# Kernel tuning notes

Measured on AMD Instinct MI355X. Metric: run time of the kernel, lower is better.

The kernel has to match this reference:

```python
import jax, jax.numpy as jnp
import numpy as np

B, N, M, E = 2, 16384, 16384, 49152
W_CHAMFER, W_EDGE = 1.0, 0.1


def setup_inputs() -> dict:
    key = jax.random.key(0)
    k1, k2, k3 = jax.random.split(key, 3)
    pred_verts = jax.random.normal(k1, (B, N, 3), dtype=jnp.float32)
    target_verts = jax.random.normal(k2, (B, M, 3), dtype=jnp.float32)
    edges = jax.random.randint(k3, (E, 2), 0, N, dtype=jnp.int64)
    return {"pred_verts": pred_verts, "target_verts": target_verts, "edges": edges}


def reference(pred_verts, target_verts, edges):
    # --- Chamfer distance (torch.cdist + bidirectional min) ---
    # Squared-distance expansion avoids materializing the B x N x M x 3 diff tensor.
    p2 = jnp.sum(pred_verts * pred_verts, axis=-1)            # [B, N]
    t2 = jnp.sum(target_verts * target_verts, axis=-1)        # [B, M]
    cross = jnp.einsum('bnd,bmd->bnm', pred_verts, target_verts)  # [B, N, M]
    d2 = p2[:, :, None] + t2[:, None, :] - 2.0 * cross
    dist = jnp.sqrt(jnp.maximum(d2, 0.0))                     # [B, N, M]
    c_loss = jnp.mean(jnp.min(dist, axis=2)) + jnp.mean(jnp.min(dist, axis=1))

    # --- Edge-length variance regularization (vectorized over batch) ---
    v1 = pred_verts[:, edges[:, 0]]                           # [B, E, 3]
    v2 = pred_verts[:, edges[:, 1]]                           # [B, E, 3]
    edge_lengths = jnp.linalg.norm(v1 - v2, axis=-1)          # [B, E]
    # torch.var defaults to unbiased (ddof=1); mean over batch == sum/B
    e_loss = jnp.mean(jnp.var(edge_lengths, axis=1, ddof=1))

    total_loss = W_CHAMFER * c_loss + W_EDGE * e_loss
    return (total_loss, c_loss, e_loss)
```

## Files before the change

kernel.cpp:

```cpp
#include <hip/hip_runtime.h>
#include <float.h>

#define B_SZ 2
#define N_SZ 16384
#define E_SZ 49152

#define TPB 512
#define WAVES (TPB / 64)
#define ROWS_PER_BLOCK 256
#define MSPLIT 4
#define MRANGE (N_SZ / MSPLIT)
#define CHUNK 512
#define NCHUNK (MRANGE / CHUNK)
#define TILES_PER_CHUNK (CHUNK / 32)

#define CH_BLOCKS (2 * (B_SZ * N_SZ / ROWS_PER_BLOCK) * MSPLIT)
#define EDGE_BLOCKS (B_SZ * E_SZ / TPB)
#define NROWS_TOT (2 * B_SZ * N_SZ)

#define PLANE_BYTES (N_SZ * 16)
#define BATCH_FRAG_BYTES (2 * PLANE_BYTES)
#define DIR_FRAG_BYTES (B_SZ * BATCH_FRAG_BYTES)
#define MINS_OFF (2 * DIR_FRAG_BYTES)
#define SUMS_OFF (MINS_OFF + NROWS_TOT * 4)

typedef short short8 __attribute__((ext_vector_type(8)));
typedef float f32x16 __attribute__((ext_vector_type(16)));

__device__ inline short f2bf(float f) {
    unsigned u = __float_as_uint(f);
    unsigned r = (u + 0x7fffu + ((u >> 16) & 1u)) >> 16;
    return (short)r;
}
__device__ inline float bf2f(short s) {
    return __uint_as_float(((unsigned)(unsigned short)s) << 16);
}

__device__ inline unsigned fmapu(float f) {
    unsigned u = __float_as_uint(f);
    return ((int)u < 0) ? ~u : (u ^ 0x80000000u);
}
__device__ inline float funmapu(unsigned v) {
    unsigned b = ((int)v < 0) ? (v ^ 0x80000000u) : ~v;
    return __uint_as_float(b);
}

__global__ __launch_bounds__(TPB) void prep(const float* __restrict__ pred,
                                            const float* __restrict__ tgt,
                                            char* __restrict__ ws) {
    int idx = blockIdx.x * TPB + threadIdx.x;
    if (blockIdx.x == 0 && threadIdx.x < 6)
        ((double*)(ws + SUMS_OFF))[threadIdx.x] = 0.0;
    if (idx < NROWS_TOT) ((unsigned*)(ws + MINS_OFF))[idx] = 0xFFFFFFFFu;
    if (idx >= 2 * B_SZ * N_SZ) return;

    const bool isTgt = idx < B_SZ * N_SZ;
    int row = isTgt ? idx : idx - B_SZ * N_SZ;
    int batch = row >> 14, pt = row & (N_SZ - 1);
    const float* src = (isTgt ? tgt : pred) + (size_t)row * 3;
    char* base = ws + (isTgt ? 0 : DIR_FRAG_BYTES) + (size_t)batch * BATCH_FRAG_BYTES;

    float tx = src[0], ty = src[1], tz = src[2];
    short hx = f2bf(tx), hy = f2bf(ty), hz = f2bf(tz);
    short lx = f2bf(tx - bf2f(hx)), ly = f2bf(ty - bf2f(hy)), lz = f2bf(tz - bf2f(hz));
    float t2 = fmaf(tx, tx, fmaf(ty, ty, tz * tz));
    short t2h = f2bf(t2), t2l = f2bf(t2 - bf2f(t2h));
    const short one = 0x3f80;

    *(short8*)(base + (size_t)pt * 16) = (short8){hx, hy, hz, hx, hy, hz, one, one};
    *(short8*)(base + PLANE_BYTES + (size_t)pt * 16) =
        (short8){lx, ly, lz, t2h, t2l, 0, 0, 0};
}

__global__ __launch_bounds__(TPB, 1) void main_kernel(
    const float* __restrict__ pred, const float* __restrict__ tgt,
    const int* __restrict__ edges, char* __restrict__ ws)
{
    __shared__ __align__(16) char sB[2][2 * CHUNK * 16];
    __shared__ float wred[WAVES], wred2[WAVES];
    double* sums = (double*)(ws + SUMS_OFF);
    unsigned* minOut = (unsigned*)(ws + MINS_OFF);
    const int lane = threadIdx.x & 63;
    const int wv = threadIdx.x >> 6;

    if (blockIdx.x >= EDGE_BLOCKS) {
        const int cb = blockIdx.x - EDGE_BLOCKS;
        const int dir = cb >> 9;
        const int rest = cb & 511;
        const int ms = rest >> 7;
        const int xb = rest & 127;
        const int batch = xb >> 6;
        const int rowInB = (xb & 63) * ROWS_PER_BLOCK;
        const float* P = dir ? tgt : pred;
        const char* fragBase = ws + (size_t)dir * DIR_FRAG_BYTES
                                  + (size_t)batch * BATCH_FRAG_BYTES;
        const int mBase = ms * MRANGE;
        const int bl = lane & 31;
        const int half = lane >> 5;

        int r = batch * N_SZ + rowInB + wv * 32 + bl;
        const float* p = P + (size_t)r * 3;
        float px = p[0], py = p[1], pz = p[2];
        float ax = -2.f * px, ay = -2.f * py, az = -2.f * pz;
        short ahx = f2bf(ax), ahy = f2bf(ay), ahz = f2bf(az);
        short alx = f2bf(ax - bf2f(ahx)), aly = f2bf(ay - bf2f(ahy)),
              alz = f2bf(az - bf2f(ahz));
        float p2 = fmaf(px, px, fmaf(py, py, pz * pz));
        short p2h = f2bf(p2), p2l = f2bf(p2 - bf2f(p2h));
        const short one = 0x3f80;
        short8 af = half == 0
            ? (short8){ahx, ahy, ahz, alx, aly, alz, p2h, p2l}
            : (short8){ahx, ahy, ahz, one, one, 0, 0, 0};

        const int t = threadIdx.x;
        float4 st0, st1;
        auto ldChunk = [&](int c) {
            const float4* s0 = (const float4*)(fragBase + (size_t)(mBase + c * CHUNK) * 16);
            const float4* s1 = (const float4*)(fragBase + PLANE_BYTES
                                               + (size_t)(mBase + c * CHUNK) * 16);
            st0 = s0[t]; st1 = s1[t];
        };
        auto wrChunk = [&](int buf) {
            float4* d = (float4*)sB[buf];
            d[t] = st0; d[t + TPB] = st1;
        };

        float nmin[16];
        #pragma unroll
        for (int e = 0; e < 16; e++) nmin[e] = FLT_MAX;
        const f32x16 zc = {0.f, 0.f, 0.f, 0.f, 0.f, 0.f, 0.f, 0.f,
                           0.f, 0.f, 0.f, 0.f, 0.f, 0.f, 0.f, 0.f};

        ldChunk(0); wrChunk(0);
        __syncthreads();

        for (int c = 0; c < NCHUNK; c++) {
            int buf = c & 1;
            if (c + 1 < NCHUNK) ldChunk(c + 1);
            const char* bp = sB[buf] + half * (CHUNK * 16) + bl * 16;
            #pragma unroll 2
            for (int mt = 0; mt < TILES_PER_CHUNK; mt += 2) {
                short8 b0 = *(const short8*)(bp + (mt * 32) * 16);
                short8 b1 = *(const short8*)(bp + (mt * 32 + 32) * 16);
                f32x16 r0 = __builtin_amdgcn_mfma_f32_32x32x16_bf16(af, b0, zc, 0, 0, 0);
                f32x16 r1 = __builtin_amdgcn_mfma_f32_32x32x16_bf16(af, b1, zc, 0, 0, 0);
                #pragma unroll
                for (int e = 0; e < 16; e++)
                    nmin[e] = fminf(fminf(r0[e], r1[e]), nmin[e]);
            }
            if (c + 1 < NCHUNK) wrChunk(buf ^ 1);
            __syncthreads();
        }

        float vals[16];
        #pragma unroll
        for (int e = 0; e < 16; e++) {
            float v = nmin[e];
            v = fminf(v, __shfl_xor(v, 1));
            v = fminf(v, __shfl_xor(v, 2));
            v = fminf(v, __shfl_xor(v, 4));
            v = fminf(v, __shfl_xor(v, 8));
            v = fminf(v, __shfl_xor(v, 16));
            vals[e] = v;
        }
        if (bl == 0) {
            int base = dir * (B_SZ * N_SZ) + batch * N_SZ + rowInB + wv * 32 + half * 4;
            #pragma unroll
            for (int e = 0; e < 16; e++) {
                int rrow = (e & 3) + 8 * (e >> 2);
                atomicMin(&minOut[base + rrow], fmapu(vals[e]));
            }
        }
    } else {
        int idx = blockIdx.x * TPB + threadIdx.x;
        int b = idx >= E_SZ;
        int e = idx - b * E_SZ;
        int2 ee = ((const int2*)edges)[e];
        const float* p0 = pred + ((size_t)b * N_SZ + (size_t)ee.x) * 3;
        const float* p1 = pred + ((size_t)b * N_SZ + (size_t)ee.y) * 3;
        float dx = p0[0] - p1[0], dy = p0[1] - p1[1], dz = p0[2] - p1[2];
        float len = sqrtf(dx * dx + dy * dy + dz * dz);
        float s = len, q = len * len;
        for (int o = 32; o > 0; o >>= 1) {
            s += __shfl_down(s, o, 64);
            q += __shfl_down(q, o, 64);
        }
        if (lane == 0) { wred[wv] = s; wred2[wv] = q; }
        __syncthreads();
        if (threadIdx.x == 0) {
            float ts = 0.f, tq = 0.f;
            #pragma unroll
            for (int w = 0; w < WAVES; w++) { ts += wred[w]; tq += wred2[w]; }
            atomicAdd(&sums[2 + 2 * b], (double)ts);
            atomicAdd(&sums[3 + 2 * b], (double)tq);
        }
    }
}

#define FIN_TPB 1024
__global__ __launch_bounds__(FIN_TPB) void final_kernel(const char* __restrict__ ws,
                                                        float* __restrict__ out) {
    const uint4* mins = (const uint4*)(ws + MINS_OFF);
    const double* sums = (const double*)(ws + SUMS_OFF);
    __shared__ double redA[FIN_TPB / 64], redB[FIN_TPB / 64];

    float sA = 0.f, sB = 0.f;
    #pragma unroll
    for (int i = 0; i < 16; i++) {
        uint4 v = mins[i * FIN_TPB + threadIdx.x];
        float s = sqrtf(fmaxf(funmapu(v.x), 0.f)) + sqrtf(fmaxf(funmapu(v.y), 0.f))
                + sqrtf(fmaxf(funmapu(v.z), 0.f)) + sqrtf(fmaxf(funmapu(v.w), 0.f));
        if (i < 8) sA += s; else sB += s;
    }
    for (int o = 32; o > 0; o >>= 1) {
        sA += __shfl_down(sA, o, 64);
        sB += __shfl_down(sB, o, 64);
    }
    int wv = threadIdx.x >> 6, ln = threadIdx.x & 63;
    if (ln == 0) { redA[wv] = (double)sA; redB[wv] = (double)sB; }
    __syncthreads();
    if (threadIdx.x == 0) {
        double tA = 0.0, tB = 0.0;
        #pragma unroll
        for (int w = 0; w < FIN_TPB / 64; w++) { tA += redA[w]; tB += redB[w]; }
        double c = tA / (double)(B_SZ * N_SZ) + tB / (double)(B_SZ * N_SZ);
        double e = 0.0;
        #pragma unroll
        for (int b = 0; b < B_SZ; b++) {
            double s = sums[2 + 2 * b], q = sums[3 + 2 * b];
            e += (q - s * s / (double)E_SZ) / (double)(E_SZ - 1);
        }
        e *= (1.0 / B_SZ);
        double tot = 1.0 * c + 0.1 * e;
        out[0] = (float)tot;
        out[1] = (float)c;
        out[2] = (float)e;
    }
}

extern "C" void kernel_launch(void* const* d_in, const int* in_sizes, int n_in,
                              void* d_out, int out_size, void* d_ws, size_t ws_size,
                              hipStream_t stream) {
    const float* pred = (const float*)d_in[0];
    const float* tgt  = (const float*)d_in[1];
    const int* edges  = (const int*)d_in[2];
    float* out = (float*)d_out;
    char* ws = (char*)d_ws;

    prep<<<dim3((2 * B_SZ * N_SZ) / TPB), TPB, 0, stream>>>(pred, tgt, ws);

    main_kernel<<<dim3(EDGE_BLOCKS + CH_BLOCKS), TPB, 0, stream>>>(
        pred, tgt, edges, ws);

    final_kernel<<<dim3(1), FIN_TPB, 0, stream>>>(ws, out);
}
```

Before: 110.0 us.

## Give each wave two row tiles sharing one B fragment per MFMA pair

The chamfer block size drops to 256 threads, and each wave now handles 64 rows as two 32-row A fragments. Each B fragment loaded from LDS feeds two MFMAs, which halves LDS reads per MFMA and doubles register-held minima. The chunk loader now stages four float4s per thread to fill the same shared buffer with fewer threads. The prep kernel keeps its 512-thread config. Edge blocks also become 256 threads, so EDGE_BLOCKS doubles and the block-index decoding may be affected.

```diff
diff --git a/kernel.cpp b/kernel.cpp
--- a/kernel.cpp
+++ b/kernel.cpp
@@ -5,7 +5,7 @@
 #define N_SZ 16384
 #define E_SZ 49152
 
-#define TPB 512
+#define TPB 256
 #define WAVES (TPB / 64)
 #define ROWS_PER_BLOCK 256
 #define MSPLIT 4
@@ -45,10 +45,10 @@
     return __uint_as_float(b);
 }
 
-__global__ __launch_bounds__(TPB) void prep(const float* __restrict__ pred,
+__global__ __launch_bounds__(512) void prep(const float* __restrict__ pred,
                                             const float* __restrict__ tgt,
                                             char* __restrict__ ws) {
-    int idx = blockIdx.x * TPB + threadIdx.x;
+    int idx = blockIdx.x * 512 + threadIdx.x;
     if (blockIdx.x == 0 && threadIdx.x < 6)
         ((double*)(ws + SUMS_OFF))[threadIdx.x] = 0.0;
     if (idx < NROWS_TOT) ((unsigned*)(ws + MINS_OFF))[idx] = 0xFFFFFFFFu;
@@ -97,37 +97,42 @@
         const int mBase = ms * MRANGE;
         const int bl = lane & 31;
         const int half = lane >> 5;
-
-        int r = batch * N_SZ + rowInB + wv * 32 + bl;
-        const float* p = P + (size_t)r * 3;
-        float px = p[0], py = p[1], pz = p[2];
-        float ax = -2.f * px, ay = -2.f * py, az = -2.f * pz;
-        short ahx = f2bf(ax), ahy = f2bf(ay), ahz = f2bf(az);
-        short alx = f2bf(ax - bf2f(ahx)), aly = f2bf(ay - bf2f(ahy)),
-              alz = f2bf(az - bf2f(ahz));
-        float p2 = fmaf(px, px, fmaf(py, py, pz * pz));
-        short p2h = f2bf(p2), p2l = f2bf(p2 - bf2f(p2h));
         const short one = 0x3f80;
-        short8 af = half == 0
-            ? (short8){ahx, ahy, ahz, alx, aly, alz, p2h, p2l}
-            : (short8){ahx, ahy, ahz, one, one, 0, 0, 0};
+
+        const int rowLocal = rowInB + wv * 64;
+        short8 af[2];
+        #pragma unroll
+        for (int t = 0; t < 2; t++) {
+            int r = batch * N_SZ + rowLocal + t * 32 + bl;
+            const float* p = P + (size_t)r * 3;
+            float px = p[0], py = p[1], pz = p[2];
+            float ax = -2.f * px, ay = -2.f * py, az = -2.f * pz;
+            short ahx = f2bf(ax), ahy = f2bf(ay), ahz = f2bf(az);
+            short alx = f2bf(ax - bf2f(ahx)), aly = f2bf(ay - bf2f(ahy)),
+                  alz = f2bf(az - bf2f(ahz));
+            float p2 = fmaf(px, px, fmaf(py, py, pz * pz));
+            short p2h = f2bf(p2), p2l = f2bf(p2 - bf2f(p2h));
+            af[t] = half == 0
+                ? (short8){ahx, ahy, ahz, alx, aly, alz, p2h, p2l}
+                : (short8){ahx, ahy, ahz, one, one, 0, 0, 0};
+        }
 
         const int t = threadIdx.x;
-        float4 st0, st1;
+        float4 st0, st1, st2, st3;
         auto ldChunk = [&](int c) {
             const float4* s0 = (const float4*)(fragBase + (size_t)(mBase + c * CHUNK) * 16);
             const float4* s1 = (const float4*)(fragBase + PLANE_BYTES
                                                + (size_t)(mBase + c * CHUNK) * 16);
-            st0 = s0[t]; st1 = s1[t];
+            st0 = s0[t]; st1 = s0[t + TPB]; st2 = s1[t]; st3 = s1[t + TPB];
         };
         auto wrChunk = [&](int buf) {
             float4* d = (float4*)sB[buf];
-            d[t] = st0; d[t + TPB] = st1;
+            d[t] = st0; d[t + TPB] = st1; d[t + 2 * TPB] = st2; d[t + 3 * TPB] = st3;
         };
 
-        float nmin[16];
-        #pragma unroll
-        for (int e = 0; e < 16; e++) nmin[e] = FLT_MAX;
+        float nmin0[16], nmin1[16];
+        #pragma unroll
+        for (int e = 0; e < 16; e++) { nmin0[e] = FLT_MAX; nmin1[e] = FLT_MAX; }
         const f32x16 zc = {0.f, 0.f, 0.f, 0.f, 0.f, 0.f, 0.f, 0.f,
                            0.f, 0.f, 0.f, 0.f, 0.f, 0.f, 0.f, 0.f};
 
@@ -139,36 +144,36 @@
             if (c + 1 < NCHUNK) ldChunk(c + 1);
             const char* bp = sB[buf] + half * (CHUNK * 16) + bl * 16;
             #pragma unroll 2
-            for (int mt = 0; mt < TILES_PER_CHUNK; mt += 2) {
+            for (int mt = 0; mt < TILES_PER_CHUNK; mt++) {
                 short8 b0 = *(const short8*)(bp + (mt * 32) * 16);
-                short8 b1 = *(const short8*)(bp + (mt * 32 + 32) * 16);
-                f32x16 r0 = __builtin_amdgcn_mfma_f32_32x32x16_bf16(af, b0, zc, 0, 0, 0);
-                f32x16 r1 = __builtin_amdgcn_mfma_f32_32x32x16_bf16(af, b1, zc, 0, 0, 0);
+                f32x16 r0 = __builtin_amdgcn_mfma_f32_32x32x16_bf16(af[0], b0, zc, 0, 0, 0);
+                f32x16 r1 = __builtin_amdgcn_mfma_f32_32x32x16_bf16(af[1], b0, zc, 0, 0, 0);
                 #pragma unroll
-                for (int e = 0; e < 16; e++)
-                    nmin[e] = fminf(fminf(r0[e], r1[e]), nmin[e]);
+                for (int e = 0; e < 16; e++) {
+                    nmin0[e] = fminf(nmin0[e], r0[e]);
+                    nmin1[e] = fminf(nmin1[e], r1[e]);
+                }
             }
             if (c + 1 < NCHUNK) wrChunk(buf ^ 1);
             __syncthreads();
         }
 
-        float vals[16];
-        #pragma unroll
-        for (int e = 0; e < 16; e++) {
-            float v = nmin[e];
-            v = fminf(v, __shfl_xor(v, 1));
-            v = fminf(v, __shfl_xor(v, 2));
-            v = fminf(v, __shfl_xor(v, 4));
-            v = fminf(v, __shfl_xor(v, 8));
-            v = fminf(v, __shfl_xor(v, 16));
-            vals[e] = v;
-        }
-        if (bl == 0) {
-            int base = dir * (B_SZ * N_SZ) + batch * N_SZ + rowInB + wv * 32 + half * 4;
+        #pragma unroll
+        for (int tt = 0; tt < 2; tt++) {
+            float* nm = tt ? nmin1 : nmin0;
+            int base = dir * (B_SZ * N_SZ) + batch * N_SZ + rowLocal + tt * 32 + half * 4;
             #pragma unroll
             for (int e = 0; e < 16; e++) {
-                int rrow = (e & 3) + 8 * (e >> 2);
-                atomicMin(&minOut[base + rrow], fmapu(vals[e]));
+                float v = nm[e];
+                v = fminf(v, __shfl_xor(v, 1));
+                v = fminf(v, __shfl_xor(v, 2));
+                v = fminf(v, __shfl_xor(v, 4));
+                v = fminf(v, __shfl_xor(v, 8));
+                v = fminf(v, __shfl_xor(v, 16));
+                if (bl == 0) {
+                    int rrow = (e & 3) + 8 * (e >> 2);
+                    atomicMin(&minOut[base + rrow], fmapu(v));
+                }
             }
         }
     } else {
@@ -247,7 +252,7 @@
     float* out = (float*)d_out;
     char* ws = (char*)d_ws;
 
-    prep<<<dim3((2 * B_SZ * N_SZ) / TPB), TPB, 0, stream>>>(pred, tgt, ws);
+    prep<<<dim3((2 * B_SZ * N_SZ) / 512), 512, 0, stream>>>(pred, tgt, ws);
 
     main_kernel<<<dim3(EDGE_BLOCKS + CH_BLOCKS), TPB, 0, stream>>>(
         pred, tgt, edges, ws);
```

After: 139.1 us. +26.4%, slower.
